# Kernel optimization log

Measured on AMD Instinct MI355X. Metric: run time of the kernel, lower is better.

## Reference

```python
import math
import jax, jax.numpy as jnp
import numpy as np

N, L, W = 64, 128, 256          # batch, num windows, window size
D, H, NL = 384, 8, 4            # d_model, heads, transformer layers
DFF = 1536
CH = [1, 4, 16, 64]             # conv channels (multiplier 4)
K = 7                            # conv kernel, pad 3, stride 1; pool k2 s2
LIN_IN = 64 * 32                # cnn_linear_size = 2048


def _pe(l, d):
    pos = np.arange(l)[:, None].astype(np.float32)
    i = np.arange(d // 2)[None, :].astype(np.float32)
    ang = pos / np.power(10000.0, 2.0 * i / d)
    pe = np.zeros((l, d), np.float32)
    pe[:, 0::2] = np.sin(ang)
    pe[:, 1::2] = np.cos(ang)
    return jnp.asarray(pe)


def _conv1d(x, w, b):
    y = jax.lax.conv_general_dilated(x, w, window_strides=(1,), padding=[(3, 3)],
                                     dimension_numbers=('NCH', 'OIH', 'NCH'))
    return y + b[None, :, None]


def _maxpool2(x):
    return jax.lax.reduce_window(x, -jnp.inf, jax.lax.max, (1, 1, 2), (1, 1, 2), 'VALID')


def _ln(x, g, b):
    m = x.mean(-1, keepdims=True)
    v = ((x - m) ** 2).mean(-1, keepdims=True)
    return (x - m) * jax.lax.rsqrt(v + 1e-5) * g + b


def setup_inputs() -> dict:
    key = jax.random.key(0)
    ks = iter(jax.random.split(key, 40))
    s = 0.02
    d = {'x': jax.random.normal(next(ks), (N, L, W), jnp.float32)}
    for i in range(3):
        d[f'conv_w{i}'] = jax.random.normal(next(ks), (CH[i + 1], CH[i], K), jnp.float32) * s
        d[f'conv_b{i}'] = jnp.zeros((CH[i + 1],), jnp.float32)
    d['embed_w'] = jax.random.normal(next(ks), (LIN_IN, D), jnp.float32) * s
    d['embed_b'] = jnp.zeros((D,), jnp.float32)
    for nm, sh in [('Wq', (NL, D, D)), ('Wk', (NL, D, D)), ('Wv', (NL, D, D)), ('Wo', (NL, D, D)),
                   ('W1', (NL, D, DFF)), ('W2', (NL, DFF, D))]:
        d[nm] = jax.random.normal(next(ks), sh, jnp.float32) * s
    for nm, sh in [('bq', (NL, D)), ('bk', (NL, D)), ('bv', (NL, D)), ('bo', (NL, D)),
                   ('b1', (NL, DFF)), ('b2', (NL, D))]:
        d[nm] = jnp.zeros(sh, jnp.float32)
    d['g1'] = jnp.ones((NL, D), jnp.float32); d['be1'] = jnp.zeros((NL, D), jnp.float32)
    d['g2'] = jnp.ones((NL, D), jnp.float32); d['be2'] = jnp.zeros((NL, D), jnp.float32)
    d['cls_w'] = jax.random.normal(next(ks), (D, 1), jnp.float32) * s
    d['cls_b'] = jnp.zeros((1,), jnp.float32)
    return d


def reference(x, conv_w0, conv_b0, conv_w1, conv_b1, conv_w2, conv_b2,
              embed_w, embed_b, Wq, bq, Wk, bk, Wv, bv, Wo, bo,
              W1, b1, W2, b2, g1, be1, g2, be2, cls_w, cls_b):
    n, l, w = x.shape
    # ---- CNN window encoder: each window -> d_model token ----
    h = x.reshape(n * l, 1, w)
    for cw, cb in ((conv_w0, conv_b0), (conv_w1, conv_b1), (conv_w2, conv_b2)):
        h = _maxpool2(jax.nn.relu(_conv1d(h, cw, cb)))
    h = h.reshape(n * l, -1)                      # (N*L, cnn_linear_size)
    h = jax.nn.relu(h @ embed_w + embed_b)        # (N*L, D)
    t = h.reshape(n, l, D) + _pe(l, D)
    # ---- transformer encoder (fast_transformers post-norm layers) ----
    E = D // H
    temp = 1.0 / math.sqrt(E)
    for i in range(Wq.shape[0]):
        q = (t @ Wq[i] + bq[i]).reshape(n, l, H, E)
        k = (t @ Wk[i] + bk[i]).reshape(n, l, H, E)
        v = (t @ Wv[i] + bv[i]).reshape(n, l, H, E)
        A = jax.nn.softmax(temp * jnp.einsum('nlhe,nshe->nhls', q, k), axis=-1)
        o = jnp.einsum('nhls,nshd->nlhd', A, v).reshape(n, l, D)
        t = _ln(t + o @ Wo[i] + bo[i], g1[i], be1[i])
        y = jax.nn.relu(t @ W1[i] + b1[i]) @ W2[i] + b2[i]
        t = _ln(t + y, g2[i], be2[i])
    # ---- classifier head: mean pool over windows -> logit ----
    return t.mean(axis=1) @ cls_w + cls_b          # (N, 1)
```

## Files before the change

kernel.cpp:

```cpp
#include <hip/hip_runtime.h>
#include <math.h>


typedef float f32x4 __attribute__((ext_vector_type(4)));
typedef short bf16x8 __attribute__((ext_vector_type(8)));
typedef short s16x4 __attribute__((ext_vector_type(4)));

__device__ __forceinline__ short f2bf(float f) {
    union { float f; unsigned u; } c; c.f = f;
    unsigned r = (c.u + 0x7FFFu + ((c.u >> 16) & 1u)) >> 16;
    return (short)r;
}
__device__ __forceinline__ float bf2f(short s) {
    union { unsigned u; float f; } c;
    c.u = ((unsigned)(unsigned short)s) << 16;
    return c.f;
}

__device__ __forceinline__ void gload_lds16(const void* g, void* l) {
    __builtin_amdgcn_global_load_lds(
        (const __attribute__((address_space(1))) unsigned int*)g,
        (__attribute__((address_space(3))) unsigned int*)l,
        16, 0, 0);
}

__global__ __launch_bounds__(384) void pe_kernel(float* __restrict__ pe) {
    int l = blockIdx.x, d = threadIdx.x;
    int i2 = d >> 1;
    float ang = (float)l * expf(-(2.0f * (float)i2 / 384.0f) * 9.210340371976184f);
    pe[l * 384 + d] = (d & 1) ? cosf(ang) : sinf(ang);
}

__global__ __launch_bounds__(256) void wcvt_kernel(
    const float* __restrict__ W, short* __restrict__ Wt, int K, int N,
    int dstOff, int srcZ, int dstZ)
{
    __shared__ float tile[32][33];
    int kb = blockIdx.x * 32, nb = blockIdx.y * 32;
    const float* Wp = W + (size_t)blockIdx.z * srcZ;
    short* Wtp = Wt + (size_t)blockIdx.z * dstZ + dstOff;
    int tx = threadIdx.x & 31, ty = threadIdx.x >> 5;
    #pragma unroll
    for (int r = ty; r < 32; r += 8)
        tile[r][tx] = Wp[(size_t)(kb + r) * N + nb + tx];
    __syncthreads();
    #pragma unroll
    for (int r = ty; r < 32; r += 8)
        Wtp[(size_t)(nb + r) * K + kb + tx] = f2bf(tile[tx][r]);
}

__global__ __launch_bounds__(256) void qkvcvt_kernel(
    const float* __restrict__ Wq, const float* __restrict__ Wk,
    const float* __restrict__ Wv, short* __restrict__ WqkvT)
{
    __shared__ float tile[32][33];
    int kb = blockIdx.x * 32, nb = blockIdx.y * 32;
    int layer = blockIdx.z / 3, which = blockIdx.z - layer * 3;
    const float* Wp = (which == 0 ? Wq : (which == 1 ? Wk : Wv)) +
                      (size_t)layer * 147456;
    short* Wtp = WqkvT + (size_t)layer * 442368 + (size_t)which * 147456;
    int tx = threadIdx.x & 31, ty = threadIdx.x >> 5;
    #pragma unroll
    for (int r = ty; r < 32; r += 8)
        tile[r][tx] = Wp[(size_t)(kb + r) * 384 + nb + tx];
    __syncthreads();
    #pragma unroll
    for (int r = ty; r < 32; r += 8)
        Wtp[(size_t)(nb + r) * 384 + kb + tx] = f2bf(tile[tx][r]);
}

__global__ __launch_bounds__(256) void w2cvt_kernel(
    const float* __restrict__ w2, short* __restrict__ w2T)
{
    int idx = blockIdx.x * 256 + threadIdx.x;
    int c = idx >> 7, r = idx & 127;
    int pr = r >> 5, q = (r >> 3) & 3, j = r & 7;
    int ci = (q & 1) * 8 + j;
    int sft = 2 * pr + (q >> 1);
    w2T[idx] = (sft < 7) ? f2bf(w2[c * 112 + ci * 7 + sft]) : (short)0;
}

__global__ __launch_bounds__(384) void biascat_kernel(
    const float* __restrict__ bq, const float* __restrict__ bk,
    const float* __restrict__ bv, float* __restrict__ bqkv)
{
    int l = blockIdx.x, j = threadIdx.x;
    bqkv[l * 1152 + j] = bq[l * 384 + j];
    bqkv[l * 1152 + 384 + j] = bk[l * 384 + j];
    bqkv[l * 1152 + 768 + j] = bv[l * 384 + j];
}

__global__ __launch_bounds__(256, 4) void cnn_kernel(
    const float* __restrict__ x,
    const float* __restrict__ w0, const float* __restrict__ b0,
    const float* __restrict__ w1, const float* __restrict__ b1,
    const short* __restrict__ w2T, const float* __restrict__ b2,
    short* __restrict__ feat)
{
    __shared__ __align__(16) char smem[26880];
    float* xs  = (float*)smem;
    float* p0  = (float*)(smem + 4224);
    short* p1T = (short*)(smem + 13056);

    int tid = threadIdx.x;
    int w = tid >> 6, lane = tid & 63;
    size_t win = (size_t)blockIdx.x * 4 + w;
    int cq = lane >> 4, cl = lane & 15;

    float* xs_w = xs + w * 264;
    float* p0_w = p0 + w * 552;
    short* p1T_w = p1T + w * 1728;

    int ca = lane & 3;
    int cb = lane & 15, g = lane >> 4;
    float w0r[7], w1r[4][7];
    float b0r = b0[ca];
    float b1r = b1[cb];
    #pragma unroll
    for (int k = 0; k < 7; ++k) w0r[k] = w0[ca * 7 + k];
    #pragma unroll
    for (int ci = 0; ci < 4; ++ci)
        #pragma unroll
        for (int k = 0; k < 7; ++k) w1r[ci][k] = w1[(cb * 4 + ci) * 7 + k];

    {
        f32x4 v = *(const f32x4*)(x + win * 256 + lane * 4);
        *(f32x4*)&xs_w[4 + lane * 4] = v;
        if (lane < 2) *(f32x4*)&xs_w[lane * 260] = (f32x4){0.f, 0.f, 0.f, 0.f};
    }

    {
        int pa = lane >> 2;
        #pragma unroll
        for (int t2 = 0; t2 < 8; ++t2) {
            int pp = t2 * 16 + pa;
            float rv[9];
            #pragma unroll
            for (int u = 0; u < 9; ++u) rv[u] = xs_w[2 * pp + u + 1];
            float a0 = b0r, a1 = b0r;
            #pragma unroll
            for (int k = 0; k < 7; ++k) {
                a0 = fmaf(w0r[k], rv[k], a0);
                a1 = fmaf(w0r[k], rv[k + 1], a1);
            }
            p0_w[ca * 138 + pp + 3] = fmaxf(fmaxf(a0, a1), 0.f);
        }
        if (lane < 4) {
            p0_w[lane * 138 + 0] = 0.f;
            p0_w[lane * 138 + 1] = 0.f;
            p0_w[lane * 138 + 2] = 0.f;
            p0_w[lane * 138 + 131] = 0.f;
            p0_w[lane * 138 + 132] = 0.f;
            p0_w[lane * 138 + 133] = 0.f;
        }
    }

    #pragma unroll
    for (int cc = 0; cc < 4; ++cc) {
        int cci = (cc + g) & 3;
        int j0 = g * 32 + cci * 8;
        float acc[8];
        #pragma unroll
        for (int m = 0; m < 8; ++m) acc[m] = b1r;
        #pragma unroll
        for (int ci = 0; ci < 4; ++ci) {
            float rv[14];
            #pragma unroll
            for (int u = 0; u < 14; ++u) rv[u] = p0_w[ci * 138 + j0 + u];
            #pragma unroll
            for (int k = 0; k < 7; ++k) {
                float ww = w1r[ci][k];
                #pragma unroll
                for (int m = 0; m < 8; ++m) acc[m] = fmaf(ww, rv[m + k], acc[m]);
            }
        }
        int po = g * 16 + cci * 4;
        #pragma unroll
        for (int m = 0; m < 4; ++m)
            p1T_w[(3 + po + m) * 24 + cb] =
                f2bf(fmaxf(fmaxf(acc[2 * m], acc[2 * m + 1]), 0.f));
    }
    {
        int* pz = (int*)p1T_w;
        if (lane < 36) pz[lane] = 0;
        if (lane < 60) pz[804 + lane] = 0;
    }
    __syncthreads();

    f32x4 acc[4][4];
    #pragma unroll
    for (int v = 0; v < 4; ++v)
        #pragma unroll
        for (int mt = 0; mt < 4; ++mt)
            acc[v][mt] = (f32x4){0.f, 0.f, 0.f, 0.f};

    {
        const short* bpb = p1T + (w * 16 + cl + (cq >> 1)) * 24 + (cq & 1) * 8;
        #pragma unroll
        for (int pr = 0; pr < 4; ++pr) {
            bf16x8 bfr[4];
            #pragma unroll
            for (int v = 0; v < 4; ++v)
                bfr[v] = *(const bf16x8*)&bpb[v * 1728 + pr * 48];
            #pragma unroll
            for (int mt = 0; mt < 4; ++mt) {
                bf16x8 af = *(const bf16x8*)&w2T[(mt * 16 + cl) * 128 +
                                                 pr * 32 + cq * 8];
                #pragma unroll
                for (int v = 0; v < 4; ++v)
                    acc[v][mt] = __builtin_amdgcn_mfma_f32_16x16x32_bf16(
                        af, bfr[v], acc[v][mt], 0, 0, 0);
            }
        }
    }

    int iev = (w * 16 + cl) >> 1;
    #pragma unroll
    for (int v = 0; v < 4; ++v) {
        short* fp = feat + ((size_t)blockIdx.x * 4 + v) * 2048;
        #pragma unroll
        for (int mt = 0; mt < 4; ++mt) {
            #pragma unroll
            for (int rg = 0; rg < 4; ++rg) {
                float vv = acc[v][mt][rg];
                float v2 = __shfl_xor(vv, 1, 64);
                if ((cl & 1) == 0) {
                    int c = mt * 16 + cq * 4 + rg;
                    float pv = fmaxf(fmaxf(vv, v2) + b2[c], 0.f);
                    fp[c * 32 + iev] = f2bf(pv);
                }
            }
        }
    }
}

template <int EPI>
__global__ __launch_bounds__(256) void gemm_bf16(
    const short* __restrict__ A, const short* __restrict__ Bt,
    const float* __restrict__ bias, const float* __restrict__ resid,
    const float* __restrict__ pe, float* __restrict__ outF,
    short* __restrict__ outB, int M, int N, int K)
{
    __shared__ short As[2][128 * 64];
    __shared__ short Bs[2][64 * 64];
    int tid = threadIdx.x;
    int w = tid >> 6, lane = tid & 63;
    int wm = w >> 1, wn = w & 1;
    int m0 = blockIdx.y * 128, n0 = blockIdx.x * 64;

    int rl = lane >> 3, sl = lane & 7;
    int cb = sl ^ rl;
    const short* aptr[4];
    const short* bptr[2];
    int arow[4], brow[2];
    #pragma unroll
    for (int l = 0; l < 4; ++l) {
        arow[l] = l * 32 + w * 8;
        aptr[l] = A + (size_t)(m0 + arow[l] + rl) * K + cb * 8;
    }
    #pragma unroll
    for (int l = 0; l < 2; ++l) {
        brow[l] = l * 32 + w * 8;
        bptr[l] = Bt + (size_t)(n0 + brow[l] + rl) * K + cb * 8;
    }

    int cq = lane >> 4, cl = lane & 15;
    f32x4 acc[4][2];
    #pragma unroll
    for (int mt = 0; mt < 4; ++mt)
        #pragma unroll
        for (int nt = 0; nt < 2; ++nt)
            acc[mt][nt] = (f32x4){0.f, 0.f, 0.f, 0.f};

    #pragma unroll
    for (int l = 0; l < 4; ++l) { gload_lds16(aptr[l], &As[0][arow[l] * 64]); aptr[l] += 64; }
    #pragma unroll
    for (int l = 0; l < 2; ++l) { gload_lds16(bptr[l], &Bs[0][brow[l] * 64]); bptr[l] += 64; }
    __syncthreads();

    int nk = K >> 6;
    for (int k = 0; k < nk; ++k) {
        int cur = k & 1;
        if (k + 1 < nk) {
            #pragma unroll
            for (int l = 0; l < 4; ++l) { gload_lds16(aptr[l], &As[cur ^ 1][arow[l] * 64]); aptr[l] += 64; }
            #pragma unroll
            for (int l = 0; l < 2; ++l) { gload_lds16(bptr[l], &Bs[cur ^ 1][brow[l] * 64]); bptr[l] += 64; }
        }
        #pragma unroll
        for (int s = 0; s < 2; ++s) {
            bf16x8 afr[4], bfr[2];
            #pragma unroll
            for (int mt = 0; mt < 4; ++mt) {
                int r = wm * 64 + mt * 16 + cl;
                int slot = (s * 4 + cq) ^ (r & 7);
                afr[mt] = *(const bf16x8*)&As[cur][r * 64 + slot * 8];
            }
            #pragma unroll
            for (int nt = 0; nt < 2; ++nt) {
                int r = wn * 32 + nt * 16 + cl;
                int slot = (s * 4 + cq) ^ (r & 7);
                bfr[nt] = *(const bf16x8*)&Bs[cur][r * 64 + slot * 8];
            }
            #pragma unroll
            for (int mt = 0; mt < 4; ++mt)
                #pragma unroll
                for (int nt = 0; nt < 2; ++nt)
                    acc[mt][nt] = __builtin_amdgcn_mfma_f32_16x16x32_bf16(
                        afr[mt], bfr[nt], acc[mt][nt], 0, 0, 0);
        }
        __syncthreads();
    }

    #pragma unroll
    for (int mt = 0; mt < 4; ++mt) {
        #pragma unroll
        for (int nt = 0; nt < 2; ++nt) {
            int col = n0 + wn * 32 + nt * 16 + cl;
            float bb = bias[col];
            #pragma unroll
            for (int rg = 0; rg < 4; ++rg) {
                int row = m0 + wm * 64 + mt * 16 + cq * 4 + rg;
                float v = acc[mt][nt][rg] + bb;
                if (EPI & 1) v = fmaxf(v, 0.f);
                if (EPI & 4) v += pe[(row & 127) * 384 + col];
                if (EPI & 2) v += resid[(size_t)row * N + col];
                if (EPI & 8) outF[(size_t)row * N + col] = v;
                if (EPI & 16) outB[(size_t)row * N + col] = f2bf(v);
            }
        }
    }
}

template <int EPI>
__global__ __launch_bounds__(256) void gemm_bf16_wide(
    const short* __restrict__ A, const short* __restrict__ Bt,
    const float* __restrict__ bias, float* __restrict__ outF,
    short* __restrict__ outB, int M, int N, int K)
{
    __shared__ short As[2][128 * 32];
    __shared__ short Bs[2][128 * 32];
    int tid = threadIdx.x;
    int w = tid >> 6, lane = tid & 63;
    int wm = w >> 1, wn = w & 1;
    int m0 = blockIdx.y * 128, n0 = blockIdx.x * 128;

    int rl = lane >> 2, sl = lane & 3;
    int cb = sl ^ (rl & 3) ^ ((rl >> 2) & 3);
    const short* aptr[2];
    const short* bptr[2];
    int srow[2];
    #pragma unroll
    for (int l = 0; l < 2; ++l) {
        srow[l] = w * 32 + l * 16;
        aptr[l] = A + (size_t)(m0 + srow[l] + rl) * K + cb * 8;
        bptr[l] = Bt + (size_t)(n0 + srow[l] + rl) * K + cb * 8;
    }

    int cq = lane >> 4, cl = lane & 15;
    f32x4 acc[4][4];
    #pragma unroll
    for (int mt = 0; mt < 4; ++mt)
        #pragma unroll
        for (int nt = 0; nt < 4; ++nt)
            acc[mt][nt] = (f32x4){0.f, 0.f, 0.f, 0.f};

    #pragma unroll
    for (int l = 0; l < 2; ++l) {
        gload_lds16(aptr[l], &As[0][srow[l] * 32]);
        gload_lds16(bptr[l], &Bs[0][srow[l] * 32]);
        aptr[l] += 32; bptr[l] += 32;
    }
    __syncthreads();

    int nk = K >> 5;
    for (int k = 0; k < nk; ++k) {
        int cur = k & 1;
        if (k + 1 < nk) {
            #pragma unroll
            for (int l = 0; l < 2; ++l) {
                gload_lds16(aptr[l], &As[cur ^ 1][srow[l] * 32]);
                gload_lds16(bptr[l], &Bs[cur ^ 1][srow[l] * 32]);
                aptr[l] += 32; bptr[l] += 32;
            }
        }
        bf16x8 afr[4], bfr[4];
        #pragma unroll
        for (int mt = 0; mt < 4; ++mt) {
            int r = wm * 64 + mt * 16 + cl;
            int slot = cq ^ (r & 3) ^ ((r >> 2) & 3);
            afr[mt] = *(const bf16x8*)&As[cur][r * 32 + slot * 8];
        }
        #pragma unroll
        for (int nt = 0; nt < 4; ++nt) {
            int r = wn * 64 + nt * 16 + cl;
            int slot = cq ^ (r & 3) ^ ((r >> 2) & 3);
            bfr[nt] = *(const bf16x8*)&Bs[cur][r * 32 + slot * 8];
        }
        #pragma unroll
        for (int mt = 0; mt < 4; ++mt)
            #pragma unroll
            for (int nt = 0; nt < 4; ++nt)
                acc[mt][nt] = __builtin_amdgcn_mfma_f32_16x16x32_bf16(
                    afr[mt], bfr[nt], acc[mt][nt], 0, 0, 0);
        __syncthreads();
    }

    #pragma unroll
    for (int mt = 0; mt < 4; ++mt) {
        #pragma unroll
        for (int nt = 0; nt < 4; ++nt) {
            int col = n0 + wn * 64 + nt * 16 + cl;
            float bb = bias[col];
            #pragma unroll
            for (int rg = 0; rg < 4; ++rg) {
                int row = m0 + wm * 64 + mt * 16 + cq * 4 + rg;
                float v = acc[mt][nt][rg] + bb;
                if (EPI & 1) v = fmaxf(v, 0.f);
                if (EPI & 8) outF[(size_t)row * N + col] = v;
                if (EPI & 16) outB[(size_t)row * N + col] = f2bf(v);
            }
        }
    }
}

__global__ __launch_bounds__(256) void gemm_ln(
    const short* __restrict__ A, const short* __restrict__ Bt,
    const float* __restrict__ bias, const float* resid,
    const float* __restrict__ g, const float* __restrict__ be,
    float* t, short* __restrict__ tb, int K)
{
    __shared__ __align__(16) char smem[51200];
    short* As = (short*)smem;
    short* Bs = (short*)(smem + 2048);

    int tid = threadIdx.x;
    int w = tid >> 6, lane = tid & 63;
    int m0 = blockIdx.x * 16;
    int rl = lane >> 3, sl = lane & 7;
    int cb = sl ^ rl;

    const short* aptr = A + (size_t)(m0 + w * 8 + rl) * K + cb * 8;
    const short* bptr[12];
    #pragma unroll
    for (int l = 0; l < 12; ++l)
        bptr[l] = Bt + (size_t)(w * 96 + l * 8 + rl) * K + cb * 8;

    int cq = lane >> 4, cl = lane & 15;
    f32x4 acc[6];
    #pragma unroll
    for (int nt = 0; nt < 6; ++nt) acc[nt] = (f32x4){0.f, 0.f, 0.f, 0.f};

    for (int k0 = 0; k0 < K; k0 += 64) {
        if (w < 2) {
            gload_lds16(aptr, &As[(w * 8) * 64]);
            aptr += 64;
        }
        #pragma unroll
        for (int l = 0; l < 12; ++l) {
            gload_lds16(bptr[l], &Bs[(w * 96 + l * 8) * 64]);
            bptr[l] += 64;
        }
        __syncthreads();
        #pragma unroll
        for (int s = 0; s < 2; ++s) {
            bf16x8 afr, bfr[6];
            {
                int r = cl;
                int slot = (s * 4 + cq) ^ (r & 7);
                afr = *(const bf16x8*)&As[r * 64 + slot * 8];
            }
            #pragma unroll
            for (int nt = 0; nt < 6; ++nt) {
                int r = w * 96 + nt * 16 + cl;
                int slot = (s * 4 + cq) ^ (r & 7);
                bfr[nt] = *(const bf16x8*)&Bs[r * 64 + slot * 8];
            }
            #pragma unroll
            for (int nt = 0; nt < 6; ++nt)
                acc[nt] = __builtin_amdgcn_mfma_f32_16x16x32_bf16(
                    afr, bfr[nt], acc[nt], 0, 0, 0);
        }
        __syncthreads();
    }

    float* yb = (float*)smem;
    #pragma unroll
    for (int nt = 0; nt < 6; ++nt) {
        int col = w * 96 + nt * 16 + cl;
        float bb = bias[col];
        #pragma unroll
        for (int rg = 0; rg < 4; ++rg) {
            int rloc = cq * 4 + rg;
            yb[rloc * 388 + col] =
                acc[nt][rg] + bb + resid[(size_t)(m0 + rloc) * 384 + col];
        }
    }
    __syncthreads();

    int rloc = tid >> 4, sub = tid & 15;
    f32x4 vals[6];
    float s = 0.f, s2 = 0.f;
    #pragma unroll
    for (int m = 0; m < 6; ++m) {
        f32x4 vv = *(const f32x4*)&yb[rloc * 388 + m * 64 + sub * 4];
        vals[m] = vv;
        #pragma unroll
        for (int j = 0; j < 4; ++j) {
            s += vv[j];
            s2 = fmaf(vv[j], vv[j], s2);
        }
    }
    s += __shfl_xor(s, 1, 64);  s2 += __shfl_xor(s2, 1, 64);
    s += __shfl_xor(s, 2, 64);  s2 += __shfl_xor(s2, 2, 64);
    s += __shfl_xor(s, 4, 64);  s2 += __shfl_xor(s2, 4, 64);
    s += __shfl_xor(s, 8, 64);  s2 += __shfl_xor(s2, 8, 64);
    float mean = s * (1.f / 384.f);
    float var = s2 * (1.f / 384.f) - mean * mean;
    float inv = rsqrtf(var + 1e-5f);

    size_t ro = (size_t)(m0 + rloc) * 384;
    #pragma unroll
    for (int m = 0; m < 6; ++m) {
        int c0 = m * 64 + sub * 4;
        f32x4 gg = *(const f32x4*)&g[c0];
        f32x4 bb = *(const f32x4*)&be[c0];
        f32x4 ov;
        s16x4 ob2;
        #pragma unroll
        for (int j = 0; j < 4; ++j) {
            float v = (vals[m][j] - mean) * inv * gg[j] + bb[j];
            ov[j] = v;
            ob2[j] = f2bf(v);
        }
        *(f32x4*)&t[ro + c0] = ov;
        *(s16x4*)&tb[ro + c0] = ob2;
    }
}

__global__ __launch_bounds__(256) void attn_kernel(
    const short* __restrict__ qkv, short* __restrict__ o)
{
    __shared__ __align__(16) short lds[23936];
    short* Vt = lds;
    short* P  = lds + 6528;

    int tid = threadIdx.x;
    int w = tid >> 6, lane = tid & 63;
    int cq = lane >> 4, cl = lane & 15;
    int n = blockIdx.x >> 3, h = blockIdx.x & 7;
    size_t base = (size_t)n * 147456 + (size_t)h * 48;
    const short* qp = qkv + base;
    const short* kp = qkv + base + 384;
    const short* vp = qkv + base + 768;

    {
        int key = tid >> 1, half = tid & 1;
        const short* vsrc = vp + (size_t)key * 1152 + half * 24;
        #pragma unroll
        for (int e4 = 0; e4 < 6; ++e4) {
            s16x4 vv = *(const s16x4*)(vsrc + e4 * 4);
            int e0 = half * 24 + e4 * 4;
            Vt[(e0 + 0) * 136 + key] = vv[0];
            Vt[(e0 + 1) * 136 + key] = vv[1];
            Vt[(e0 + 2) * 136 + key] = vv[2];
            Vt[(e0 + 3) * 136 + key] = vv[3];
        }
    }

    const bf16x8 zf = (bf16x8){0, 0, 0, 0, 0, 0, 0, 0};
    bf16x8 qf[2][2];
    #pragma unroll
    for (int mt = 0; mt < 2; ++mt) {
        const short* qrow = qp + (size_t)(w * 32 + mt * 16 + cl) * 1152;
        qf[mt][0] = *(const bf16x8*)(qrow + cq * 8);
        qf[mt][1] = (cq < 2) ? *(const bf16x8*)(qrow + 32 + cq * 8) : zf;
    }

    f32x4 sacc[2][8];
    #pragma unroll
    for (int mt = 0; mt < 2; ++mt)
        #pragma unroll
        for (int kt = 0; kt < 8; ++kt)
            sacc[mt][kt] = (f32x4){0.f, 0.f, 0.f, 0.f};

    #pragma unroll
    for (int kt = 0; kt < 8; ++kt) {
        const short* krow = kp + (size_t)(kt * 16 + cl) * 1152;
        bf16x8 kf0 = *(const bf16x8*)(krow + cq * 8);
        bf16x8 kf1 = (cq < 2) ? *(const bf16x8*)(krow + 32 + cq * 8) : zf;
        #pragma unroll
        for (int mt = 0; mt < 2; ++mt) {
            sacc[mt][kt] = __builtin_amdgcn_mfma_f32_16x16x32_bf16(
                qf[mt][0], kf0, sacc[mt][kt], 0, 0, 0);
            sacc[mt][kt] = __builtin_amdgcn_mfma_f32_16x16x32_bf16(
                qf[mt][1], kf1, sacc[mt][kt], 0, 0, 0);
        }
    }
    __syncthreads();

    const float temp = 0.14433756729740643f;
    short* Pw = P + w * 4352;
    float denom[2][4];
    #pragma unroll
    for (int mt = 0; mt < 2; ++mt) {
        #pragma unroll
        for (int rg = 0; rg < 4; ++rg) {
            float m0 = sacc[mt][0][rg];
            #pragma unroll
            for (int kt = 1; kt < 8; ++kt) m0 = fmaxf(m0, sacc[mt][kt][rg]);
            m0 = fmaxf(m0, __shfl_xor(m0, 1, 64));
            m0 = fmaxf(m0, __shfl_xor(m0, 2, 64));
            m0 = fmaxf(m0, __shfl_xor(m0, 4, 64));
            m0 = fmaxf(m0, __shfl_xor(m0, 8, 64));
            int row = mt * 16 + cq * 4 + rg;
            float se = 0.f;
            #pragma unroll
            for (int kt = 0; kt < 8; ++kt) {
                float p = __expf(temp * (sacc[mt][kt][rg] - m0));
                se += p;
                Pw[row * 136 + kt * 16 + cl] = f2bf(p);
            }
            se += __shfl_xor(se, 1, 64);
            se += __shfl_xor(se, 2, 64);
            se += __shfl_xor(se, 4, 64);
            se += __shfl_xor(se, 8, 64);
            denom[mt][rg] = se;
        }
    }

    f32x4 oacc[2][3];
    #pragma unroll
    for (int mt = 0; mt < 2; ++mt)
        #pragma unroll
        for (int nt = 0; nt < 3; ++nt)
            oacc[mt][nt] = (f32x4){0.f, 0.f, 0.f, 0.f};

    #pragma unroll
    for (int ks = 0; ks < 4; ++ks) {
        bf16x8 paf[2];
        #pragma unroll
        for (int mt = 0; mt < 2; ++mt)
            paf[mt] = *(const bf16x8*)&Pw[(mt * 16 + cl) * 136 + ks * 32 + cq * 8];
        #pragma unroll
        for (int nt = 0; nt < 3; ++nt) {
            bf16x8 vf = *(const bf16x8*)&Vt[(nt * 16 + cl) * 136 + ks * 32 + cq * 8];
            #pragma unroll
            for (int mt = 0; mt < 2; ++mt)
                oacc[mt][nt] = __builtin_amdgcn_mfma_f32_16x16x32_bf16(
                    paf[mt], vf, oacc[mt][nt], 0, 0, 0);
        }
    }

    #pragma unroll
    for (int mt = 0; mt < 2; ++mt) {
        #pragma unroll
        for (int rg = 0; rg < 4; ++rg) {
            float inv = 1.f / denom[mt][rg];
            int qrow = w * 32 + mt * 16 + cq * 4 + rg;
            short* op = o + ((size_t)n * 128 + qrow) * 384 + h * 48;
            #pragma unroll
            for (int nt = 0; nt < 3; ++nt)
                op[nt * 16 + cl] = f2bf(oacc[mt][nt][rg] * inv);
        }
    }
}

__global__ __launch_bounds__(384) void head_kernel(
    const float* __restrict__ t, const float* __restrict__ cls_w,
    const float* __restrict__ cls_b, float* __restrict__ out)
{
    int n = blockIdx.x, d = threadIdx.x;
    float s = 0.f;
    for (int l = 0; l < 128; ++l) s += t[((size_t)n * 128 + l) * 384 + d];
    float p = s * (1.f / 128.f) * cls_w[d];
    #pragma unroll
    for (int off = 32; off > 0; off >>= 1) p += __shfl_xor(p, off, 64);
    __shared__ float red[6];
    if ((threadIdx.x & 63) == 0) red[threadIdx.x >> 6] = p;
    __syncthreads();
    if (threadIdx.x == 0) {
        float tot = red[0] + red[1] + red[2] + red[3] + red[4] + red[5];
        out[n] = tot + cls_b[0];
    }
}

extern "C" void kernel_launch(void* const* d_in, const int* in_sizes, int n_in,
                              void* d_out, int out_size, void* d_ws, size_t ws_size,
                              hipStream_t stream) {
    (void)n_in; (void)out_size; (void)ws_size;
    const float* x   = (const float*)d_in[0];
    const float* cw0 = (const float*)d_in[1];
    const float* cb0 = (const float*)d_in[2];
    const float* cw1 = (const float*)d_in[3];
    const float* cb1 = (const float*)d_in[4];
    const float* cw2 = (const float*)d_in[5];
    const float* cb2 = (const float*)d_in[6];
    const float* ew  = (const float*)d_in[7];
    const float* eb  = (const float*)d_in[8];
    bool dict_order = (in_sizes[10] == 589824);
    const float *Wq, *Wk, *Wv, *Wo, *W1, *W2, *bq, *bk, *bv, *bo, *b1, *b2;
    if (dict_order) {
        Wq = (const float*)d_in[9];  Wk = (const float*)d_in[10];
        Wv = (const float*)d_in[11]; Wo = (const float*)d_in[12];
        W1 = (const float*)d_in[13]; W2 = (const float*)d_in[14];
        bq = (const float*)d_in[15]; bk = (const float*)d_in[16];
        bv = (const float*)d_in[17]; bo = (const float*)d_in[18];
        b1 = (const float*)d_in[19]; b2 = (const float*)d_in[20];
    } else {
        Wq = (const float*)d_in[9];  bq = (const float*)d_in[10];
        Wk = (const float*)d_in[11]; bk = (const float*)d_in[12];
        Wv = (const float*)d_in[13]; bv = (const float*)d_in[14];
        Wo = (const float*)d_in[15]; bo = (const float*)d_in[16];
        W1 = (const float*)d_in[17]; b1 = (const float*)d_in[18];
        W2 = (const float*)d_in[19]; b2 = (const float*)d_in[20];
    }
    const float* g1  = (const float*)d_in[21];
    const float* be1 = (const float*)d_in[22];
    const float* g2  = (const float*)d_in[23];
    const float* be2 = (const float*)d_in[24];
    const float* clw = (const float*)d_in[25];
    const float* clb = (const float*)d_in[26];

    char* wp = (char*)d_ws;
    float* pe    = (float*)wp; wp += 196608;
    short* featb = (short*)wp; wp += 33554432;
    float* t     = (float*)wp; wp += 12582912;
    short* tb    = (short*)wp; wp += 6291456;
    short* qkvb  = (short*)wp; wp += 18874368;
    short* ob    = (short*)wp; wp += 6291456;
    short* ewT   = (short*)wp; wp += 1572864;
    short* WqkvT = (short*)wp; wp += 3538944;
    short* WoT   = (short*)wp; wp += 1179648;
    short* W1T   = (short*)wp; wp += 4718592;
    short* W2T   = (short*)wp; wp += 4718592;
    float* bqkv  = (float*)wp; wp += 18432;
    short* w2T   = (short*)wp; wp += 16384;
    short* hb    = featb;

    const int ROWS = 8192;

    pe_kernel<<<128, 384, 0, stream>>>(pe);
    wcvt_kernel<<<dim3(64, 12, 1), 256, 0, stream>>>(ew, ewT, 2048, 384, 0, 0, 0);
    qkvcvt_kernel<<<dim3(12, 12, 12), 256, 0, stream>>>(Wq, Wk, Wv, WqkvT);
    wcvt_kernel<<<dim3(12, 12, 4), 256, 0, stream>>>(Wo, WoT, 384, 384, 0, 147456, 147456);
    wcvt_kernel<<<dim3(12, 48, 4), 256, 0, stream>>>(W1, W1T, 384, 1536, 0, 589824, 589824);
    wcvt_kernel<<<dim3(48, 12, 4), 256, 0, stream>>>(W2, W2T, 1536, 384, 0, 589824, 589824);
    biascat_kernel<<<4, 384, 0, stream>>>(bq, bk, bv, bqkv);
    w2cvt_kernel<<<32, 256, 0, stream>>>(cw2, w2T);
    cnn_kernel<<<2048, 256, 0, stream>>>(x, cw0, cb0, cw1, cb1, w2T, cb2, featb);

    gemm_bf16<29><<<dim3(6, 64), 256, 0, stream>>>(featb, ewT, eb, nullptr, pe,
                                                   t, tb, ROWS, 384, 2048);
    for (int i = 0; i < 4; ++i) {
        const short* WqkvTi = WqkvT + (size_t)i * 442368;
        const short* WoTi = WoT + (size_t)i * 147456;
        const short* W1Ti = W1T + (size_t)i * 589824;
        const short* W2Ti = W2T + (size_t)i * 589824;
        gemm_bf16_wide<16><<<dim3(9, 64), 256, 0, stream>>>(tb, WqkvTi,
            bqkv + i * 1152, nullptr, qkvb, ROWS, 1152, 384);
        attn_kernel<<<512, 256, 0, stream>>>(qkvb, ob);
        gemm_ln<<<512, 256, 0, stream>>>(ob, WoTi, bo + i * 384, t,
            g1 + i * 384, be1 + i * 384, t, tb, 384);
        gemm_bf16_wide<17><<<dim3(12, 64), 256, 0, stream>>>(tb, W1Ti,
            b1 + i * 1536, nullptr, hb, ROWS, 1536, 384);
        gemm_ln<<<512, 256, 0, stream>>>(hb, W2Ti, b2 + i * 384, t,
            g2 + i * 384, be2 + i * 384, t, tb, 1536);
    }
    head_kernel<<<64, 384, 0, stream>>>(t, clw, clb, (float*)d_out);
}
```

Before: 630.4 us.

## Double gemm_ln row tile to 32 with 512 threads and LDS double-buffering

The fused GEMM+LayerNorm kernel now processes 32 rows per block with 8 waves instead of 16 rows with 4 waves. Each wave computes a 2x3 MFMA tile over a 48-column slice. This halves how often the full weight matrix is re-read across blocks. K-slices are double-buffered in LDS so the next tile's global-to-LDS load overlaps the current MFMAs. The cost is about 104 KB of LDS per block, which limits occupancy to roughly one block per CU, and half as many blocks in the grid.

```diff
diff --git a/kernel.cpp b/kernel.cpp
--- a/kernel.cpp
+++ b/kernel.cpp
@@ -424,76 +424,95 @@
     }
 }
 
-__global__ __launch_bounds__(256) void gemm_ln(
+__global__ __launch_bounds__(512) void gemm_ln(
     const short* __restrict__ A, const short* __restrict__ Bt,
     const float* __restrict__ bias, const float* resid,
     const float* __restrict__ g, const float* __restrict__ be,
     float* t, short* __restrict__ tb, int K)
 {
-    __shared__ __align__(16) char smem[51200];
-    short* As = (short*)smem;
-    short* Bs = (short*)(smem + 2048);
+    __shared__ __align__(16) char smem[106496];
+    short* As0 = (short*)smem;
+    short* Bs0 = (short*)(smem + 8192);
 
     int tid = threadIdx.x;
     int w = tid >> 6, lane = tid & 63;
-    int m0 = blockIdx.x * 16;
+    int m0 = blockIdx.x * 32;
     int rl = lane >> 3, sl = lane & 7;
     int cb = sl ^ rl;
 
-    const short* aptr = A + (size_t)(m0 + w * 8 + rl) * K + cb * 8;
-    const short* bptr[12];
-    #pragma unroll
-    for (int l = 0; l < 12; ++l)
-        bptr[l] = Bt + (size_t)(w * 96 + l * 8 + rl) * K + cb * 8;
+    const short* aptr = A + (size_t)(m0 + (w & 3) * 8 + rl) * K + cb * 8;
+    const short* bptr[6];
+    #pragma unroll
+    for (int l = 0; l < 6; ++l)
+        bptr[l] = Bt + (size_t)(w * 48 + l * 8 + rl) * K + cb * 8;
 
     int cq = lane >> 4, cl = lane & 15;
-    f32x4 acc[6];
-    #pragma unroll
-    for (int nt = 0; nt < 6; ++nt) acc[nt] = (f32x4){0.f, 0.f, 0.f, 0.f};
-
-    for (int k0 = 0; k0 < K; k0 += 64) {
-        if (w < 2) {
-            gload_lds16(aptr, &As[(w * 8) * 64]);
-            aptr += 64;
-        }
-        #pragma unroll
-        for (int l = 0; l < 12; ++l) {
-            gload_lds16(bptr[l], &Bs[(w * 96 + l * 8) * 64]);
-            bptr[l] += 64;
-        }
-        __syncthreads();
+    f32x4 acc[2][3];
+    #pragma unroll
+    for (int mt = 0; mt < 2; ++mt)
+        #pragma unroll
+        for (int nt = 0; nt < 3; ++nt)
+            acc[mt][nt] = (f32x4){0.f, 0.f, 0.f, 0.f};
+
+    if (w < 4) { gload_lds16(aptr, &As0[(w * 8) * 64]); aptr += 64; }
+    #pragma unroll
+    for (int l = 0; l < 6; ++l) {
+        gload_lds16(bptr[l], &Bs0[(w * 48 + l * 8) * 64]);
+        bptr[l] += 64;
+    }
+    __syncthreads();
+
+    int nk = K >> 6;
+    for (int k = 0; k < nk; ++k) {
+        int cur = k & 1;
+        if (k + 1 < nk) {
+            if (w < 4) { gload_lds16(aptr, &As0[(cur ^ 1) * 2048 + (w * 8) * 64]); aptr += 64; }
+            #pragma unroll
+            for (int l = 0; l < 6; ++l) {
+                gload_lds16(bptr[l], &Bs0[(cur ^ 1) * 24576 + (w * 48 + l * 8) * 64]);
+                bptr[l] += 64;
+            }
+        }
+        const short* As = As0 + cur * 2048;
+        const short* Bs = Bs0 + cur * 24576;
         #pragma unroll
         for (int s = 0; s < 2; ++s) {
-            bf16x8 afr, bfr[6];
-            {
-                int r = cl;
+            bf16x8 afr[2], bfr[3];
+            #pragma unroll
+            for (int mt = 0; mt < 2; ++mt) {
+                int r = mt * 16 + cl;
                 int slot = (s * 4 + cq) ^ (r & 7);
-                afr = *(const bf16x8*)&As[r * 64 + slot * 8];
-            }
-            #pragma unroll
-            for (int nt = 0; nt < 6; ++nt) {
-                int r = w * 96 + nt * 16 + cl;
+                afr[mt] = *(const bf16x8*)&As[r * 64 + slot * 8];
+            }
+            #pragma unroll
+            for (int nt = 0; nt < 3; ++nt) {
+                int r = w * 48 + nt * 16 + cl;
                 int slot = (s * 4 + cq) ^ (r & 7);
                 bfr[nt] = *(const bf16x8*)&Bs[r * 64 + slot * 8];
             }
             #pragma unroll
-            for (int nt = 0; nt < 6; ++nt)
-                acc[nt] = __builtin_amdgcn_mfma_f32_16x16x32_bf16(
-                    afr, bfr[nt], acc[nt], 0, 0, 0);
+            for (int mt = 0; mt < 2; ++mt)
+                #pragma unroll
+                for (int nt = 0; nt < 3; ++nt)
+                    acc[mt][nt] = __builtin_amdgcn_mfma_f32_16x16x32_bf16(
+                        afr[mt], bfr[nt], acc[mt][nt], 0, 0, 0);
         }
         __syncthreads();
     }
 
     float* yb = (float*)smem;
     #pragma unroll
-    for (int nt = 0; nt < 6; ++nt) {
-        int col = w * 96 + nt * 16 + cl;
-        float bb = bias[col];
-        #pragma unroll
-        for (int rg = 0; rg < 4; ++rg) {
-            int rloc = cq * 4 + rg;
-            yb[rloc * 388 + col] =
-                acc[nt][rg] + bb + resid[(size_t)(m0 + rloc) * 384 + col];
+    for (int mt = 0; mt < 2; ++mt) {
+        #pragma unroll
+        for (int nt = 0; nt < 3; ++nt) {
+            int col = w * 48 + nt * 16 + cl;
+            float bb = bias[col];
+            #pragma unroll
+            for (int rg = 0; rg < 4; ++rg) {
+                int rloc = mt * 16 + cq * 4 + rg;
+                yb[rloc * 388 + col] =
+                    acc[mt][nt][rg] + bb + resid[(size_t)(m0 + rloc) * 384 + col];
+            }
         }
     }
     __syncthreads();
@@ -760,11 +779,11 @@
         gemm_bf16_wide<16><<<dim3(9, 64), 256, 0, stream>>>(tb, WqkvTi,
             bqkv + i * 1152, nullptr, qkvb, ROWS, 1152, 384);
         attn_kernel<<<512, 256, 0, stream>>>(qkvb, ob);
-        gemm_ln<<<512, 256, 0, stream>>>(ob, WoTi, bo + i * 384, t,
+        gemm_ln<<<256, 512, 0, stream>>>(ob, WoTi, bo + i * 384, t,
             g1 + i * 384, be1 + i * 384, t, tb, 384);
         gemm_bf16_wide<17><<<dim3(12, 64), 256, 0, stream>>>(tb, W1Ti,
             b1 + i * 1536, nullptr, hb, ROWS, 1536, 384);
-        gemm_ln<<<512, 256, 0, stream>>>(hb, W2Ti, b2 + i * 384, t,
+        gemm_ln<<<256, 512, 0, stream>>>(hb, W2Ti, b2 + i * 384, t,
             g2 + i * 384, be2 + i * 384, t, tb, 1536);
     }
     head_kernel<<<64, 384, 0, stream>>>(t, clw, clb, (float*)d_out);
```

Result: no change. 621.5 us (-1.4%).
